# Kernel optimization log

Measured on AMD Instinct MI355X. Metric: run time of the kernel, lower is better.

Reference implementation:

```python
import jax, jax.numpy as jnp
import numpy as np

B, H, W = 16, 544, 960
DISP_MAX = 64.0


def setup_inputs() -> dict:
    key = jax.random.key(0)
    k1, k2, k3, k4 = jax.random.split(key, 4)
    dl = jax.random.uniform(k1, (B, 1, H, W), dtype=jnp.float32) * DISP_MAX
    seg_r = jax.random.normal(k2, (B, 1, H, W), dtype=jnp.float32)
    dlgt = jax.random.uniform(k3, (B, H, W), dtype=jnp.float32) * DISP_MAX
    lgt = jax.random.normal(k4, (B, 1, H, W), dtype=jnp.float32)
    return {"dl": dl, "seg_r": seg_r, "dlgt": dlgt, "lgt": lgt}


def _warp(x, disp):
    """Disparity warp: sample x at (h, w - disp) with horizontal bilinear
    interpolation and zeros padding (grid_sample equivalent; y is untouched
    so the vertical weights collapse to 1)."""
    Bc, C, Hc, Wc = x.shape
    cols = jnp.arange(Wc, dtype=x.dtype)  # [W]
    sx = cols[None, None, None, :] - disp  # [B,1,H,W] sampling x-coord
    x0 = jnp.floor(sx)
    wx = sx - x0  # fractional part, carries grad wrt disp
    x0i = x0.astype(jnp.int32)
    x1i = x0i + 1
    v0m = ((x0i >= 0) & (x0i < Wc)).astype(x.dtype)
    v1m = ((x1i >= 0) & (x1i < Wc)).astype(x.dtype)
    x0c = jnp.clip(x0i, 0, Wc - 1)
    x1c = jnp.clip(x1i, 0, Wc - 1)
    # gather along width; C == 1 broadcasts against disp's channel dim
    g0 = jnp.take_along_axis(x, jnp.broadcast_to(x0c, x.shape), axis=-1)
    g1 = jnp.take_along_axis(x, jnp.broadcast_to(x1c, x.shape), axis=-1)
    return (1.0 - wx) * g0 * v0m + wx * g1 * v1m


def _smooth_l1(d):
    ad = jnp.abs(d)
    return jnp.where(ad < 1.0, 0.5 * d * d, ad - 0.5)


def reference(dl, seg_r, dlgt, lgt):
    mask = lgt > 0  # [B,1,H,W] bool
    mf = mask.astype(dl.dtype)
    cnt = mf.sum()
    recon_l = jax.nn.sigmoid(_warp(seg_r, dl))
    # masked-mean smooth L1 == mean over boolean-selected elements
    loss_recon = (_smooth_l1(recon_l - lgt) * mf).sum() / cnt
    loss = (_smooth_l1(dl - dlgt[:, None, :, :]) * mf).sum() / cnt
    loss = jnp.where(jnp.isnan(loss), jnp.zeros_like(loss), loss)
    return loss + 0.5 * loss_recon
```

## Files before the change

kernel.cpp:

```cpp
#include <hip/hip_runtime.h>
#include <math.h>

#define W 960
#define W4 240
#define NROWS (16 * 544)
#define ROWS_PB 4
#define NBLOCKS (NROWS / ROWS_PB)
#define TPB 320
#define ITERS 3
#define LDS_STRIDE 964
#define PBV4 (ROWS_PB * W4)

__device__ __forceinline__ float smooth_l1f(float d) {
    float ad = fabsf(d);
    return ad < 1.0f ? 0.5f * d * d : ad - 0.5f;
}

__global__ __launch_bounds__(TPB) void loss_kernel(
    const float* __restrict__ dl,
    const float* __restrict__ seg_r,
    const float* __restrict__ dlgt,
    const float* __restrict__ lgt,
    double* __restrict__ ws)
{
    __shared__ float srow[ROWS_PB * LDS_STRIDE];
    const int tid   = threadIdx.x;
    const int base4 = blockIdx.x * PBV4;

    float4 stg[ITERS];
    #pragma unroll
    for (int j = 0; j < ITERS; ++j)
        stg[j] = ((const float4*)seg_r)[base4 + tid + j * TPB];

    float4 dv4[ITERS], lv4[ITERS], tv4[ITERS];
    #pragma unroll
    for (int j = 0; j < ITERS; ++j) {
        int g = base4 + tid + j * TPB;
        dv4[j] = ((const float4*)dl)[g];
        lv4[j] = ((const float4*)lgt)[g];
        tv4[j] = ((const float4*)dlgt)[g];
    }

    #pragma unroll
    for (int j = 0; j < ITERS; ++j) {
        int t = tid + j * TPB;
        int r = t / W4;
        int c = t - r * W4;
        *(float4*)&srow[r * LDS_STRIDE + (c << 2)] = stg[j];
    }
    __syncthreads();

    float cnt = 0.f, s_loss = 0.f, s_recon = 0.f;
    #pragma unroll
    for (int j = 0; j < ITERS; ++j) {
        int t  = tid + j * TPB;
        int r  = t / W4;
        int c4 = t - r * W4;
        const float* __restrict__ lrow = &srow[r * LDS_STRIDE];
        float dv[4] = {dv4[j].x, dv4[j].y, dv4[j].z, dv4[j].w};
        float lv[4] = {lv4[j].x, lv4[j].y, lv4[j].z, lv4[j].w};
        float tv[4] = {tv4[j].x, tv4[j].y, tv4[j].z, tv4[j].w};
        #pragma unroll
        for (int k = 0; k < 4; ++k) {
            float m = lv[k] > 0.f ? 1.f : 0.f;
            cnt += m;
            float d = dv[k];
            s_loss += m * smooth_l1f(d - tv[k]);

            float sx  = (float)((c4 << 2) + k) - d;
            float x0f = floorf(sx);
            float wx  = sx - x0f;
            int x0 = (int)x0f;
            int x1 = x0 + 1;
            float m0 = (x0 >= 0 && x0 < W) ? 1.f : 0.f;
            float m1 = (x1 >= 0 && x1 < W) ? 1.f : 0.f;
            int x0c = min(max(x0, 0), W - 1);
            int x1c = min(max(x1, 0), W - 1);
            float g0 = lrow[x0c] * m0;
            float g1 = lrow[x1c] * m1;
            float wv = fmaf(wx, g1 - g0, g0);
            float recon = 1.f / (1.f + __expf(-wv));
            s_recon += m * smooth_l1f(recon - lv[k]);
        }
    }

    double dc = (double)cnt, dlo = (double)s_loss, dre = (double)s_recon;
    for (int off = 32; off > 0; off >>= 1) {
        dc  += __shfl_down(dc,  off, 64);
        dlo += __shfl_down(dlo, off, 64);
        dre += __shfl_down(dre, off, 64);
    }
    __shared__ double sh[3][TPB / 64];
    int lane = tid & 63, wid = tid >> 6;
    if (lane == 0) { sh[0][wid] = dc; sh[1][wid] = dlo; sh[2][wid] = dre; }
    __syncthreads();

    if (tid == 0) {
        double c = 0, l = 0, r = 0;
        #pragma unroll
        for (int j = 0; j < TPB / 64; ++j) { c += sh[0][j]; l += sh[1][j]; r += sh[2][j]; }
        double* slot = ws + blockIdx.x * 4;
        slot[0] = c; slot[1] = l; slot[2] = r;
    }
}

__global__ __launch_bounds__(256) void finalize_kernel(
    const double* __restrict__ ws, float* __restrict__ out)
{
    double c = 0, l = 0, r = 0;
    for (int i = threadIdx.x; i < NBLOCKS; i += 256) {
        const double* slot = ws + i * 4;
        c += slot[0]; l += slot[1]; r += slot[2];
    }
    for (int off = 32; off > 0; off >>= 1) {
        c += __shfl_down(c, off, 64);
        l += __shfl_down(l, off, 64);
        r += __shfl_down(r, off, 64);
    }
    __shared__ double sh[3][4];
    int lane = threadIdx.x & 63, wid = threadIdx.x >> 6;
    if (lane == 0) { sh[0][wid] = c; sh[1][wid] = l; sh[2][wid] = r; }
    __syncthreads();
    if (threadIdx.x == 0) {
        double cc = 0, ll = 0, rr = 0;
        #pragma unroll
        for (int j = 0; j < 4; ++j) { cc += sh[0][j]; ll += sh[1][j]; rr += sh[2][j]; }
        double loss = ll / cc;
        if (isnan(loss)) loss = 0.0;
        out[0] = (float)(loss + 0.5 * (rr / cc));
    }
}

extern "C" void kernel_launch(void* const* d_in, const int* in_sizes, int n_in,
                              void* d_out, int out_size, void* d_ws, size_t ws_size,
                              hipStream_t stream) {
    const float* dl    = (const float*)d_in[0];
    const float* seg_r = (const float*)d_in[1];
    const float* dlgt  = (const float*)d_in[2];
    const float* lgt   = (const float*)d_in[3];
    double* ws = (double*)d_ws;

    loss_kernel<<<NBLOCKS, TPB, 0, stream>>>(dl, seg_r, dlgt, lgt, ws);
    finalize_kernel<<<1, 256, 0, stream>>>(ws, (float*)d_out);
}
```

Baseline: 156.8 us.

## Stage all four inputs into LDS via direct global-to-LDS async loads

Replaces per-thread register loads of seg_r, dl, lgt and dlgt with __builtin_amdgcn_global_load_lds transfers that copy all four arrays straight into LDS, then reads the per-element operands back from LDS. This skips the register round-trip for the staged row and aims for more bytes in flight per wave. The gather is also reworked to clamp a single base index and read adjacent pairs, selecting g0/g1 with a compare. LDS use grows to 4x4x960 floats (about 61 KB) per block, which may cut occupancy, and the padded row stride is dropped.

```diff
diff --git a/kernel.cpp b/kernel.cpp
--- a/kernel.cpp
+++ b/kernel.cpp
@@ -2,14 +2,13 @@
 #include <math.h>
 
 #define W 960
-#define W4 240
 #define NROWS (16 * 544)
 #define ROWS_PB 4
 #define NBLOCKS (NROWS / ROWS_PB)
 #define TPB 320
 #define ITERS 3
-#define LDS_STRIDE 964
-#define PBV4 (ROWS_PB * W4)
+#define ELEMS_PB (ROWS_PB * W)
+#define PBV4 (ELEMS_PB / 4)
 
 __device__ __forceinline__ float smooth_l1f(float d) {
     float ad = fabsf(d);
@@ -23,30 +22,23 @@
     const float* __restrict__ lgt,
     double* __restrict__ ws)
 {
-    __shared__ float srow[ROWS_PB * LDS_STRIDE];
-    const int tid   = threadIdx.x;
-    const int base4 = blockIdx.x * PBV4;
-
-    float4 stg[ITERS];
-    #pragma unroll
-    for (int j = 0; j < ITERS; ++j)
-        stg[j] = ((const float4*)seg_r)[base4 + tid + j * TPB];
-
-    float4 dv4[ITERS], lv4[ITERS], tv4[ITERS];
-    #pragma unroll
-    for (int j = 0; j < ITERS; ++j) {
-        int g = base4 + tid + j * TPB;
-        dv4[j] = ((const float4*)dl)[g];
-        lv4[j] = ((const float4*)lgt)[g];
-        tv4[j] = ((const float4*)dlgt)[g];
-    }
+    __shared__ float lds_all[4 * ELEMS_PB];
+    const int tid       = threadIdx.x;
+    const int wave      = tid >> 6;
+    const int lane      = tid & 63;
+    const int blockBase = blockIdx.x * ELEMS_PB;
 
     #pragma unroll
-    for (int j = 0; j < ITERS; ++j) {
-        int t = tid + j * TPB;
-        int r = t / W4;
-        int c = t - r * W4;
-        *(float4*)&srow[r * LDS_STRIDE + (c << 2)] = stg[j];
+    for (int r = 0; r < 4; ++r) {
+        const float* src = (r == 0) ? seg_r : (r == 1) ? dl : (r == 2) ? lgt : dlgt;
+        #pragma unroll
+        for (int i = 0; i < 3; ++i) {
+            int off = (wave + i * 5) * 256;
+            __builtin_amdgcn_global_load_lds(
+                (const __attribute__((address_space(1))) void*)(src + blockBase + off + lane * 4),
+                (__attribute__((address_space(3))) void*)&lds_all[r * ELEMS_PB + off],
+                16, 0, 0);
+        }
     }
     __syncthreads();
 
@@ -54,12 +46,15 @@
     #pragma unroll
     for (int j = 0; j < ITERS; ++j) {
         int t  = tid + j * TPB;
-        int r  = t / W4;
-        int c4 = t - r * W4;
-        const float* __restrict__ lrow = &srow[r * LDS_STRIDE];
-        float dv[4] = {dv4[j].x, dv4[j].y, dv4[j].z, dv4[j].w};
-        float lv[4] = {lv4[j].x, lv4[j].y, lv4[j].z, lv4[j].w};
-        float tv[4] = {tv4[j].x, tv4[j].y, tv4[j].z, tv4[j].w};
+        int r  = t / 240;
+        int c4 = t - r * 240;
+        const float* __restrict__ lrow = &lds_all[r * W];
+        float4 d4 = *(const float4*)&lds_all[1 * ELEMS_PB + 4 * t];
+        float4 l4 = *(const float4*)&lds_all[2 * ELEMS_PB + 4 * t];
+        float4 t4 = *(const float4*)&lds_all[3 * ELEMS_PB + 4 * t];
+        float dv[4] = {d4.x, d4.y, d4.z, d4.w};
+        float lv[4] = {l4.x, l4.y, l4.z, l4.w};
+        float tv[4] = {t4.x, t4.y, t4.z, t4.w};
         #pragma unroll
         for (int k = 0; k < 4; ++k) {
             float m = lv[k] > 0.f ? 1.f : 0.f;
@@ -74,10 +69,12 @@
             int x1 = x0 + 1;
             float m0 = (x0 >= 0 && x0 < W) ? 1.f : 0.f;
             float m1 = (x1 >= 0 && x1 < W) ? 1.f : 0.f;
-            int x0c = min(max(x0, 0), W - 1);
-            int x1c = min(max(x1, 0), W - 1);
-            float g0 = lrow[x0c] * m0;
-            float g1 = lrow[x1c] * m1;
+            int xb = min(max(x0, 0), W - 2);
+            float p0 = lrow[xb];
+            float p1 = lrow[xb + 1];
+            bool  c  = (x0 == xb);
+            float g0 = (c ? p0 : p1) * m0;
+            float g1 = (c ? p1 : p0) * m1;
             float wv = fmaf(wx, g1 - g0, g0);
             float recon = 1.f / (1.f + __expf(-wv));
             s_recon += m * smooth_l1f(recon - lv[k]);
@@ -91,8 +88,7 @@
         dre += __shfl_down(dre, off, 64);
     }
     __shared__ double sh[3][TPB / 64];
-    int lane = tid & 63, wid = tid >> 6;
-    if (lane == 0) { sh[0][wid] = dc; sh[1][wid] = dlo; sh[2][wid] = dre; }
+    if (lane == 0) { sh[0][wave] = dc; sh[1][wave] = dlo; sh[2][wave] = dre; }
     __syncthreads();
 
     if (tid == 0) {
```

Result: slower. 165.6 us (+5.6%).

## Replace LDS row staging with grid-stride loop and direct global gathers

Applied to the files above, without the earlier changes.

Drops the per-block shared-memory staging of seg_r rows and instead gathers the two warp samples straight from global memory (relying on L1/L2 caching). The launch becomes a fixed 2048-block grid-stride loop of 256 threads, and the streamed inputs dl, lgt and dlgt use nontemporal loads. This removes the LDS write, barrier and one-shot-per-block structure, at the cost of scattered global gathers that may miss in cache and longer per-thread loops.

```diff
diff --git a/kernel.cpp b/kernel.cpp
--- a/kernel.cpp
+++ b/kernel.cpp
@@ -2,14 +2,12 @@
 #include <math.h>
 
 #define W 960
-#define W4 240
-#define NROWS (16 * 544)
-#define ROWS_PB 4
-#define NBLOCKS (NROWS / ROWS_PB)
-#define TPB 320
-#define ITERS 3
-#define LDS_STRIDE 964
-#define PBV4 (ROWS_PB * W4)
+#define NTOT (16 * 544 * 960)
+#define N4 (NTOT / 4)
+#define TPB 256
+#define NBLOCKS 2048
+
+typedef float vfloat4 __attribute__((ext_vector_type(4)));
 
 __device__ __forceinline__ float smooth_l1f(float d) {
     float ad = fabsf(d);
@@ -23,51 +21,27 @@
     const float* __restrict__ lgt,
     double* __restrict__ ws)
 {
-    __shared__ float srow[ROWS_PB * LDS_STRIDE];
-    const int tid   = threadIdx.x;
-    const int base4 = blockIdx.x * PBV4;
+    const int tid = threadIdx.x;
+    float cnt = 0.f, s_loss = 0.f, s_recon = 0.f;
 
-    float4 stg[ITERS];
-    #pragma unroll
-    for (int j = 0; j < ITERS; ++j)
-        stg[j] = ((const float4*)seg_r)[base4 + tid + j * TPB];
+    for (int i4 = blockIdx.x * TPB + tid; i4 < N4; i4 += NBLOCKS * TPB) {
+        int i  = i4 << 2;
+        int w0 = i % W;
+        const float* __restrict__ row = seg_r + (i - w0);
 
-    float4 dv4[ITERS], lv4[ITERS], tv4[ITERS];
-    #pragma unroll
-    for (int j = 0; j < ITERS; ++j) {
-        int g = base4 + tid + j * TPB;
-        dv4[j] = ((const float4*)dl)[g];
-        lv4[j] = ((const float4*)lgt)[g];
-        tv4[j] = ((const float4*)dlgt)[g];
-    }
+        vfloat4 d4 = __builtin_nontemporal_load((const vfloat4*)dl   + i4);
+        vfloat4 l4 = __builtin_nontemporal_load((const vfloat4*)lgt  + i4);
+        vfloat4 t4 = __builtin_nontemporal_load((const vfloat4*)dlgt + i4);
 
-    #pragma unroll
-    for (int j = 0; j < ITERS; ++j) {
-        int t = tid + j * TPB;
-        int r = t / W4;
-        int c = t - r * W4;
-        *(float4*)&srow[r * LDS_STRIDE + (c << 2)] = stg[j];
-    }
-    __syncthreads();
-
-    float cnt = 0.f, s_loss = 0.f, s_recon = 0.f;
-    #pragma unroll
-    for (int j = 0; j < ITERS; ++j) {
-        int t  = tid + j * TPB;
-        int r  = t / W4;
-        int c4 = t - r * W4;
-        const float* __restrict__ lrow = &srow[r * LDS_STRIDE];
-        float dv[4] = {dv4[j].x, dv4[j].y, dv4[j].z, dv4[j].w};
-        float lv[4] = {lv4[j].x, lv4[j].y, lv4[j].z, lv4[j].w};
-        float tv[4] = {tv4[j].x, tv4[j].y, tv4[j].z, tv4[j].w};
         #pragma unroll
         for (int k = 0; k < 4; ++k) {
-            float m = lv[k] > 0.f ? 1.f : 0.f;
+            float lv = l4[k];
+            float m = lv > 0.f ? 1.f : 0.f;
             cnt += m;
-            float d = dv[k];
-            s_loss += m * smooth_l1f(d - tv[k]);
+            float d = d4[k];
+            s_loss += m * smooth_l1f(d - t4[k]);
 
-            float sx  = (float)((c4 << 2) + k) - d;
+            float sx  = (float)(w0 + k) - d;
             float x0f = floorf(sx);
             float wx  = sx - x0f;
             int x0 = (int)x0f;
@@ -76,11 +50,11 @@
             float m1 = (x1 >= 0 && x1 < W) ? 1.f : 0.f;
             int x0c = min(max(x0, 0), W - 1);
             int x1c = min(max(x1, 0), W - 1);
-            float g0 = lrow[x0c] * m0;
-            float g1 = lrow[x1c] * m1;
+            float g0 = row[x0c] * m0;
+            float g1 = row[x1c] * m1;
             float wv = fmaf(wx, g1 - g0, g0);
             float recon = 1.f / (1.f + __expf(-wv));
-            s_recon += m * smooth_l1f(recon - lv[k]);
+            s_recon += m * smooth_l1f(recon - lv);
         }
     }
 
```

Result: faster. 149.1 us (-4.9%).
